# Optimization experiments

Hardware: AMD Instinct MI355X
Metric: run time of the kernel (lower is better)

## Reference

```python
import jax, jax.numpy as jnp
import numpy as np
import math

B, T, C = 4, 2048, 2048
H, D = 16, 128
DH = D // 2  # 64 rotation planes
OMEGA_SCALE = 16.0
EPS = 1e-5


def setup_inputs() -> dict:
    key = jax.random.key(0)
    ks = jax.random.split(key, 8)
    w_std = 1.0 / math.sqrt(C)
    x = jax.random.normal(ks[0], (B, T, C), dtype=jnp.float32)
    Wq = jax.random.normal(ks[1], (C, C), dtype=jnp.float32) * w_std
    Wk = jax.random.normal(ks[2], (C, C), dtype=jnp.float32) * w_std
    Wv = jax.random.normal(ks[3], (C, C), dtype=jnp.float32) * w_std
    # c_proj init std = 0.5/sqrt(n_embd)/sqrt(n_layer), n_layer=24
    Wo = jax.random.normal(ks[4], (C, C), dtype=jnp.float32) * (0.5 / math.sqrt(C) / math.sqrt(24))
    # omega_proj: weight init zeros, bias = softplus_inverse(0.001); perturb weight slightly for a nontrivial phase
    w_omega = jax.random.normal(ks[5], (1, C), dtype=jnp.float32) * 0.01
    b_omega = jnp.full((1,), math.log(math.expm1(0.001)), dtype=jnp.float32)
    # log_freq initialized from RoPE inverse frequencies, base 10000
    inv_freq = 1.0 / (10000.0 ** (np.arange(0, D, 2, dtype=np.float32) / D))
    log_freq = jnp.asarray(np.log(inv_freq), dtype=jnp.float32)
    q_gamma = jnp.ones((D,), dtype=jnp.float32)
    k_gamma = jnp.ones((D,), dtype=jnp.float32)
    return {"x": x, "Wq": Wq, "Wk": Wk, "Wv": Wv, "Wo": Wo,
            "w_omega": w_omega, "b_omega": b_omega, "log_freq": log_freq,
            "q_gamma": q_gamma, "k_gamma": k_gamma}


def _rmsnorm(t, gamma):
    return t * jax.lax.rsqrt(jnp.mean(t * t, axis=-1, keepdims=True) + EPS) * gamma


def reference(x, Wq, Wk, Wv, Wo, w_omega, b_omega, log_freq, q_gamma, k_gamma):
    # cumulative contextual phase: omega = sigmoid(omega_proj(x)/scale); phi_t = sum_{tau<t} omega_tau
    omega = jax.nn.sigmoid((x @ w_omega.T + b_omega).astype(jnp.float32) / OMEGA_SCALE)  # (B,T,1)
    phi = jnp.cumsum(omega, axis=1) - omega                                              # (B,T,1)

    q = (x @ Wq.T).reshape(B, T, H, D)
    k = (x @ Wk.T).reshape(B, T, H, D)
    v = (x @ Wv.T).reshape(B, T, H, D)

    # shared-across-heads frequencies theta_j; angles (B,T,1,DH) broadcast over heads
    freq = jnp.exp(log_freq)                       # (DH,)
    angles = phi[..., None] * freq                 # (B,T,1,DH)
    cos = jnp.cos(angles)
    sin = jnp.sin(angles)

    def rotate(t):
        t1, t2 = t[..., :DH], t[..., DH:]
        return jnp.concatenate([t1 * cos + t2 * sin, -t1 * sin + t2 * cos], axis=-1)

    q = rotate(q)
    k = rotate(k)
    q = _rmsnorm(q, q_gamma)
    k = _rmsnorm(k, k_gamma)

    # causal SDPA, scale 1/sqrt(D)
    scores = jnp.einsum('bthd,bshd->bhts', q, k) / math.sqrt(D)   # (B,H,T,T)
    mask = jnp.tril(jnp.ones((T, T), dtype=bool))
    scores = jnp.where(mask, scores, jnp.finfo(scores.dtype).min)
    probs = jax.nn.softmax(scores, axis=-1)
    y = jnp.einsum('bhts,bshd->bthd', probs, v)                   # (B,T,H,D)
    return y.reshape(B, T, H * D) @ Wo.T
```

## Files before the change

kernel.cpp:

```cpp
#include <hip/hip_runtime.h>
#include <math.h>

typedef __bf16 bf16;
typedef __bf16 bf16x8 __attribute__((ext_vector_type(8)));
typedef __bf16 bf16x4v __attribute__((ext_vector_type(4)));
typedef float f32x4 __attribute__((ext_vector_type(4)));

#define NB 4
#define NT 2048
#define NC 2048
#define NH 16
#define ND 128
#define NROW (NB*NT)

#define GLD16(g, l) __builtin_amdgcn_global_load_lds( \
    (__attribute__((address_space(1))) void*)(g), \
    (__attribute__((address_space(3))) void*)(l), 16, 0, 0)

__global__ void cvtx_omega_kernel(const float* __restrict__ x, bf16* __restrict__ xb,
                                  const float* __restrict__ w_om, const float* __restrict__ b_om,
                                  float* __restrict__ omega) {
  int row = blockIdx.x;
  const float4* xr = reinterpret_cast<const float4*>(x + (size_t)row * NC);
  const float4* wr = reinterpret_cast<const float4*>(w_om);
  bf16x4v* ob = reinterpret_cast<bf16x4v*>(xb + (size_t)row * NC);
  float sum = 0.f;
  for (int i = threadIdx.x; i < NC/4; i += 256) {
    float4 a = xr[i], b = wr[i];
    sum += a.x*b.x + a.y*b.y + a.z*b.z + a.w*b.w;
    bf16x4v o;
    o[0] = (bf16)a.x; o[1] = (bf16)a.y; o[2] = (bf16)a.z; o[3] = (bf16)a.w;
    ob[i] = o;
  }
  for (int m = 32; m; m >>= 1) sum += __shfl_xor(sum, m);
  __shared__ float wsum[4];
  if ((threadIdx.x & 63) == 0) wsum[threadIdx.x >> 6] = sum;
  __syncthreads();
  if (threadIdx.x == 0) {
    float d = wsum[0] + wsum[1] + wsum[2] + wsum[3] + b_om[0];
    omega[row] = 1.f / (1.f + expf(-d * (1.f/16.f)));
  }
}

__global__ void cvt_kernel(const float* __restrict__ in, bf16* __restrict__ out, int n4) {
  int stride = gridDim.x * blockDim.x;
  for (int i = blockIdx.x * blockDim.x + threadIdx.x; i < n4; i += stride) {
    float4 v = reinterpret_cast<const float4*>(in)[i];
    bf16x4v o;
    o[0] = (bf16)v.x; o[1] = (bf16)v.y; o[2] = (bf16)v.z; o[3] = (bf16)v.w;
    reinterpret_cast<bf16x4v*>(out)[i] = o;
  }
}

__global__ void scan_kernel(const float* __restrict__ omega, float* __restrict__ phi) {
  int b = blockIdx.x;
  const float* om = omega + (size_t)b * NT;
  float* ph = phi + (size_t)b * NT;
  int t = threadIdx.x;
  float v[8]; float s = 0.f;
  #pragma unroll
  for (int j = 0; j < 8; j++) { v[j] = om[t*8 + j]; s += v[j]; }
  __shared__ float totals[256];
  __shared__ double base_sh[256];
  totals[t] = s;
  __syncthreads();
  if (t == 0) {
    double run = 0.0;
    for (int i = 0; i < 256; i++) { base_sh[i] = run; run += (double)totals[i]; }
  }
  __syncthreads();
  double run = base_sh[t];
  #pragma unroll
  for (int j = 0; j < 8; j++) { ph[t*8 + j] = (float)run; run += (double)v[j]; }
}

__global__ void sincos_kernel(const float* __restrict__ phi, const float* __restrict__ log_freq,
                              float* __restrict__ cos_t, float* __restrict__ sin_t) {
  int i = blockIdx.x * 256 + threadIdx.x;
  int row = i >> 6, dd = i & 63;
  float f = expf(log_freq[dd]);
  float a = phi[row] * f;
  float si, co;
  sincosf(a, &si, &co);
  cos_t[i] = co;
  sin_t[i] = si;
}

template<int MODE>
__global__ __launch_bounds__(512, 2)
void gemm256(const bf16* __restrict__ Ag, const bf16* __restrict__ Bg,
             void* __restrict__ Cout,
             const float* __restrict__ cos_t, const float* __restrict__ sin_t,
             const float* __restrict__ gamma, float outscale) {
  constexpr int NKT = NC / 64;
  __shared__ bf16 Als[2][256 * 64];
  __shared__ bf16 Bls[2][256 * 64];
  const int t = threadIdx.x;
  const int lane = t & 63, lg = lane >> 4, l15 = lane & 15;
  const int wid = t >> 6, wm = wid >> 1, wn = wid & 1;
  const int bid = blockIdx.x;
  const int wg = (bid & 7) * 32 + (bid >> 3);
  const int m0 = (wg >> 3) * 256, n0 = (wg & 7) * 256;

  const size_t K2 = (size_t)NC * 2;
  const int scol = ((t & 7) * 16) ^ (((t >> 3) & 7) << 4);
  const char* aS = (const char*)Ag + (size_t)(m0 + (t >> 3)) * K2 + scol;
  const char* bS = (const char*)Bg + (size_t)(n0 + (t >> 3)) * K2 + scol;

  const int colk0 = (lg * 16) ^ ((l15 & 7) << 4);
  const int colk[2] = { colk0, colk0 ^ 64 };
  const int arow = (wm * 64 + l15) * 128;
  const int brow = (wn * 128 + l15) * 128;

  f32x4 acc[4][8] = {};

#define STAGE_TA(kt, d) do { \
    const char* sa_ = aS + (size_t)(kt) * 128; \
    char* da_ = (char*)&Als[d][0] + t * 16; \
    GLD16(sa_,            da_); \
    GLD16(sa_ +  64*K2,   da_ + 8192); \
    GLD16(sa_ + 128*K2,   da_ + 16384); \
    GLD16(sa_ + 192*K2,   da_ + 24576); \
  } while(0)
#define STAGE_TB(kt, d) do { \
    const char* sb_ = bS + (size_t)(kt) * 128; \
    char* db_ = (char*)&Bls[d][0] + t * 16; \
    GLD16(sb_,            db_); \
    GLD16(sb_ +  64*K2,   db_ + 8192); \
    GLD16(sb_ + 128*K2,   db_ + 16384); \
    GLD16(sb_ + 192*K2,   db_ + 24576); \
  } while(0)

  STAGE_TA(0, 0); STAGE_TB(0, 0);
  asm volatile("s_waitcnt vmcnt(0)" ::: "memory");
  __builtin_amdgcn_s_barrier();
  asm volatile("" ::: "memory");

  bf16x8 aC[2][2], bC[4][2];
  for (int kt = 0; kt < NKT; kt++) {
    const int d = kt & 1;
    const char* Ab = (const char*)&Als[d][0];
    const char* Bb = (const char*)&Bls[d][0];
    const bool pf = (kt + 1 < NKT);

    #pragma unroll
    for (int i = 0; i < 2; i++)
      #pragma unroll
      for (int kk = 0; kk < 2; kk++)
        aC[i][kk] = *(const bf16x8*)(Ab + arow + (i*16)*128 + colk[kk]);
    #pragma unroll
    for (int j = 0; j < 4; j++)
      #pragma unroll
      for (int kk = 0; kk < 2; kk++)
        bC[j][kk] = *(const bf16x8*)(Bb + brow + (j*16)*128 + colk[kk]);
    if (pf) STAGE_TA(kt+1, d^1);
    __builtin_amdgcn_s_barrier();
    asm volatile("s_waitcnt lgkmcnt(0)");
    __builtin_amdgcn_s_setprio(1);
    #pragma unroll
    for (int kk = 0; kk < 2; kk++)
      #pragma unroll
      for (int i = 0; i < 2; i++)
        #pragma unroll
        for (int j = 0; j < 4; j++)
          acc[i][j] = __builtin_amdgcn_mfma_f32_16x16x32_bf16(aC[i][kk], bC[j][kk], acc[i][j], 0,0,0);
    __builtin_amdgcn_s_setprio(0);

    #pragma unroll
    for (int i = 0; i < 2; i++)
      #pragma unroll
      for (int kk = 0; kk < 2; kk++)
        aC[i][kk] = *(const bf16x8*)(Ab + arow + ((32 + i*16))*128 + colk[kk]);
    if (pf) STAGE_TB(kt+1, d^1);
    __builtin_amdgcn_s_barrier();
    asm volatile("s_waitcnt lgkmcnt(0)");
    __builtin_amdgcn_s_setprio(1);
    #pragma unroll
    for (int kk = 0; kk < 2; kk++)
      #pragma unroll
      for (int i = 0; i < 2; i++)
        #pragma unroll
        for (int j = 0; j < 4; j++)
          acc[2+i][j] = __builtin_amdgcn_mfma_f32_16x16x32_bf16(aC[i][kk], bC[j][kk], acc[2+i][j], 0,0,0);
    __builtin_amdgcn_s_setprio(0);

    #pragma unroll
    for (int j = 0; j < 4; j++)
      #pragma unroll
      for (int kk = 0; kk < 2; kk++)
        bC[j][kk] = *(const bf16x8*)(Bb + brow + ((64 + j*16))*128 + colk[kk]);
    __builtin_amdgcn_s_barrier();
    asm volatile("s_waitcnt lgkmcnt(0)");
    __builtin_amdgcn_s_setprio(1);
    #pragma unroll
    for (int kk = 0; kk < 2; kk++)
      #pragma unroll
      for (int i = 0; i < 2; i++)
        #pragma unroll
        for (int j = 0; j < 4; j++)
          acc[2+i][4+j] = __builtin_amdgcn_mfma_f32_16x16x32_bf16(aC[i][kk], bC[j][kk], acc[2+i][4+j], 0,0,0);
    __builtin_amdgcn_s_setprio(0);

    #pragma unroll
    for (int i = 0; i < 2; i++)
      #pragma unroll
      for (int kk = 0; kk < 2; kk++)
        aC[i][kk] = *(const bf16x8*)(Ab + arow + (i*16)*128 + colk[kk]);
    __builtin_amdgcn_s_barrier();
    asm volatile("s_waitcnt lgkmcnt(0)");
    __builtin_amdgcn_s_setprio(1);
    #pragma unroll
    for (int kk = 0; kk < 2; kk++)
      #pragma unroll
      for (int i = 0; i < 2; i++)
        #pragma unroll
        for (int j = 0; j < 4; j++)
          acc[i][4+j] = __builtin_amdgcn_mfma_f32_16x16x32_bf16(aC[i][kk], bC[j][kk], acc[i][4+j], 0,0,0);
    __builtin_amdgcn_s_setprio(0);

    asm volatile("s_waitcnt vmcnt(0)" ::: "memory");
    __builtin_amdgcn_s_barrier();
    asm volatile("" ::: "memory");
  }
#undef STAGE_TA
#undef STAGE_TB

  if constexpr (MODE == 0) {
    bf16* out = (bf16*)Cout;
    #pragma unroll
    for (int mi = 0; mi < 4; mi++) {
      #pragma unroll
      for (int r = 0; r < 4; r++) {
        int m = m0 + wm*64 + mi*16 + lg*4 + r;
        float ss = 0.f;
        #pragma unroll
        for (int nj = 0; nj < 8; nj++) { float v = acc[mi][nj][r]; ss += v*v; }
        ss += __shfl_xor(ss, 1); ss += __shfl_xor(ss, 2);
        ss += __shfl_xor(ss, 4); ss += __shfl_xor(ss, 8);
        float scale = rsqrtf(ss * (1.f/128.f) + 1e-5f) * outscale;
        size_t rowb = (size_t)m * NC + n0 + wn*128;
        size_t tabb = (size_t)m * 64;
        #pragma unroll
        for (int nj = 0; nj < 4; nj++) {
          int dd = nj*16 + l15;
          float c = cos_t[tabb + dd];
          float s = sin_t[tabb + dd];
          float t1 = acc[mi][nj][r], t2 = acc[mi][nj+4][r];
          float o1 = (t1*c + t2*s) * scale * gamma[dd];
          float o2 = (t2*c - t1*s) * scale * gamma[dd + 64];
          out[rowb + dd] = (bf16)o1;
          out[rowb + dd + 64] = (bf16)o2;
        }
      }
    }
  } else if constexpr (MODE == 1) {
    bf16* vt = (bf16*)Cout;
    const int h = (n0 + wn*128) >> 7;
    #pragma unroll
    for (int mi = 0; mi < 4; mi++) {
      #pragma unroll
      for (int r = 0; r < 4; r++) {
        int m = m0 + wm*64 + mi*16 + lg*4 + r;
        int bidx = m >> 11, tt = m & (NT-1);
        size_t hb = (((size_t)bidx * NH + h) * ND) * NT + tt;
        #pragma unroll
        for (int nj = 0; nj < 8; nj++) {
          int d = nj*16 + l15;
          vt[hb + (size_t)d * NT] = (bf16)acc[mi][nj][r];
        }
      }
    }
  } else {
    float* out = (float*)Cout;
    #pragma unroll
    for (int mi = 0; mi < 4; mi++) {
      #pragma unroll
      for (int r = 0; r < 4; r++) {
        int m = m0 + wm*64 + mi*16 + lg*4 + r;
        size_t rowb = (size_t)m * NC + n0 + wn*128;
        #pragma unroll
        for (int nj = 0; nj < 8; nj++)
          out[rowb + nj*16 + l15] = acc[mi][nj][r];
      }
    }
  }
}

__global__ __launch_bounds__(512, 2)
void fa_kernel(const bf16* __restrict__ Qg, const bf16* __restrict__ Kg,
               const bf16* __restrict__ Vt, bf16* __restrict__ Og) {
  __shared__ bf16 Kls[2][64 * 128];
  __shared__ bf16 Vls[128 * 64];
  __shared__ bf16 Pls[8][32 * 64];
  const int t = threadIdx.x, w = t >> 6, lane = t & 63, lg = lane >> 4, l15 = lane & 15;
  const int bh = blockIdx.x;
  const int qb = (gridDim.y - 1) - blockIdx.y;
  const size_t qkbase = (size_t)(bh >> 4) * NT * NC + (size_t)(bh & 15) * ND;
  const size_t vbase  = (size_t)bh * ND * NT;
  const int q0 = qb * 256 + w * 32;

  bf16x8 qf[2][4];
  #pragma unroll
  for (int mt = 0; mt < 2; mt++)
    #pragma unroll
    for (int kc = 0; kc < 4; kc++)
      qf[mt][kc] = *reinterpret_cast<const bf16x8*>(
          Qg + qkbase + (size_t)(q0 + mt*16 + l15) * NC + kc*32 + lg*8);

  f32x4 oacc[2][8] = {};
  f32x4 lacc[2] = {};
  float m_run[2][4];
  #pragma unroll
  for (int mt = 0; mt < 2; mt++)
    #pragma unroll
    for (int r = 0; r < 4; r++) m_run[mt][r] = -1e30f;

  bf16x8 vone;
  #pragma unroll
  for (int i = 0; i < 8; i++) vone[i] = (bf16)1.0f;

  const int kinS = ((t & 15) * 16) ^ (((t >> 4) & 7) << 4);
  const char* ksrc0 = (const char*)(Kg + qkbase) + (size_t)(t >> 4) * (NC*2) + kinS;
  const int vinS = ((t & 7) * 16) ^ (((t >> 3) & 7) << 4);
  const char* vsrc0 = (const char*)(Vt + vbase) + (size_t)(t >> 3) * (NT*2) + vinS;

#define STAGE_K(kt, dd) do { \
    const char* ks_ = ksrc0 + (size_t)(kt) * 64 * (NC*2); \
    char* kd_ = (char*)&Kls[dd][0] + t * 16; \
    GLD16(ks_,                        kd_); \
    GLD16(ks_ + (size_t)32 * NC * 2,  kd_ + 8192); \
  } while(0)
#define STAGE_V(kt) do { \
    const char* vs_ = vsrc0 + (size_t)(kt) * 128; \
    char* vd_ = (char*)&Vls[0] + t * 16; \
    GLD16(vs_,                        vd_); \
    GLD16(vs_ + (size_t)64 * NT * 2,  vd_ + 8192); \
  } while(0)

  const int ntiles = 4 * qb + 4;
  STAGE_K(0, 0);
  __syncthreads();

  for (int kt = 0; kt < ntiles; kt++) {
    const int d = kt & 1;
    const int kv0 = kt * 64;
    if (kt + 1 < ntiles) STAGE_K(kt + 1, d ^ 1);
    STAGE_V(kt);

    const bool active = (q0 + 31 >= kv0);
    if (active) {
      f32x4 s[2][4] = {};
      __builtin_amdgcn_s_setprio(1);
      #pragma unroll
      for (int kc = 0; kc < 4; kc++) {
        bf16x8 kf[4];
        const int swz = ((kc*64 + lg*16) ^ ((l15 & 7) << 4));
        #pragma unroll
        for (int nt = 0; nt < 4; nt++)
          kf[nt] = *reinterpret_cast<const bf16x8*>((const char*)&Kls[d][0] + (nt*16 + l15) * 256 + swz);
        #pragma unroll
        for (int mt = 0; mt < 2; mt++)
          #pragma unroll
          for (int nt = 0; nt < 4; nt++)
            s[mt][nt] = __builtin_amdgcn_mfma_f32_16x16x32_bf16(qf[mt][kc], kf[nt], s[mt][nt], 0, 0, 0);
      }
      __builtin_amdgcn_s_setprio(0);

      if (kv0 + 63 > q0) {
        #pragma unroll
        for (int mt = 0; mt < 2; mt++)
          #pragma unroll
          for (int nt = 0; nt < 4; nt++) {
            int kv = kv0 + nt*16 + l15;
            #pragma unroll
            for (int r = 0; r < 4; r++)
              if (kv > q0 + mt*16 + lg*4 + r) s[mt][nt][r] = -1e30f;
          }
      }

      float tmax[2][4];
      #pragma unroll
      for (int mt = 0; mt < 2; mt++)
        #pragma unroll
        for (int r = 0; r < 4; r++) {
          float tm = fmaxf(fmaxf(s[mt][0][r], s[mt][1][r]), fmaxf(s[mt][2][r], s[mt][3][r]));
          tm = fmaxf(tm, __shfl_xor(tm, 1));
          tm = fmaxf(tm, __shfl_xor(tm, 2));
          tm = fmaxf(tm, __shfl_xor(tm, 4));
          tm = fmaxf(tm, __shfl_xor(tm, 8));
          tmax[mt][r] = tm;
        }

      int ok = 1;
      #pragma unroll
      for (int mt = 0; mt < 2; mt++)
        #pragma unroll
        for (int r = 0; r < 4; r++) ok &= (tmax[mt][r] <= m_run[mt][r] + 8.0f);
      if (!__all(ok)) {
        #pragma unroll
        for (int mt = 0; mt < 2; mt++) {
          f32x4 alv;
          #pragma unroll
          for (int r = 0; r < 4; r++) {
            float mn = fmaxf(m_run[mt][r], tmax[mt][r]);
            alv[r] = exp2f(m_run[mt][r] - mn);
            m_run[mt][r] = mn;
          }
          #pragma unroll
          for (int dt = 0; dt < 8; dt++) {
            f32x4 o = oacc[mt][dt];
            o[0] *= alv[0]; o[1] *= alv[1]; o[2] *= alv[2]; o[3] *= alv[3];
            oacc[mt][dt] = o;
          }
          f32x4 lv = lacc[mt];
          lv[0] *= alv[0]; lv[1] *= alv[1]; lv[2] *= alv[2]; lv[3] *= alv[3];
          lacc[mt] = lv;
        }
      }

      char* pw = (char*)&Pls[w][0];
      #pragma unroll
      for (int mt = 0; mt < 2; mt++)
        #pragma unroll
        for (int r = 0; r < 4; r++) {
          float p0 = exp2f(s[mt][0][r] - m_run[mt][r]);
          float p1 = exp2f(s[mt][1][r] - m_run[mt][r]);
          float p2 = exp2f(s[mt][2][r] - m_run[mt][r]);
          float p3 = exp2f(s[mt][3][r] - m_run[mt][r]);
          int qrow = mt*16 + lg*4 + r;
          int rb = qrow * 128, cX = (qrow & 7) << 4;
          *(bf16*)(pw + rb + ((       2*l15) ^ cX)) = (bf16)p0;
          *(bf16*)(pw + rb + (( 32 +  2*l15) ^ cX)) = (bf16)p1;
          *(bf16*)(pw + rb + (( 64 +  2*l15) ^ cX)) = (bf16)p2;
          *(bf16*)(pw + rb + (( 96 +  2*l15) ^ cX)) = (bf16)p3;
        }
    }

    asm volatile("s_waitcnt vmcnt(0)" ::: "memory");
    __builtin_amdgcn_s_barrier();
    asm volatile("" ::: "memory");

    if (active) {
      char* pw = (char*)&Pls[w][0];
      bf16x8 pf[2][2];
      #pragma unroll
      for (int mt = 0; mt < 2; mt++)
        #pragma unroll
        for (int kc2 = 0; kc2 < 2; kc2++)
          pf[mt][kc2] = *reinterpret_cast<const bf16x8*>(
              pw + (mt*16 + l15) * 128 + ((kc2*64 + lg*16) ^ ((l15 & 7) << 4)));
      __builtin_amdgcn_s_setprio(1);
      #pragma unroll
      for (int kc2 = 0; kc2 < 2; kc2++) {
        #pragma unroll
        for (int mt = 0; mt < 2; mt++)
          lacc[mt] = __builtin_amdgcn_mfma_f32_16x16x32_bf16(pf[mt][kc2], vone, lacc[mt], 0, 0, 0);
        const int swz = ((kc2*64 + lg*16) ^ ((l15 & 7) << 4));
        #pragma unroll
        for (int dt = 0; dt < 8; dt++) {
          bf16x8 vf = *reinterpret_cast<const bf16x8*>((const char*)&Vls[0] + (dt*16 + l15) * 128 + swz);
          #pragma unroll
          for (int mt = 0; mt < 2; mt++)
            oacc[mt][dt] = __builtin_amdgcn_mfma_f32_16x16x32_bf16(pf[mt][kc2], vf, oacc[mt][dt], 0, 0, 0);
        }
      }
      __builtin_amdgcn_s_setprio(0);
    }

    __syncthreads();
  }
#undef STAGE_K
#undef STAGE_V

  #pragma unroll
  for (int mt = 0; mt < 2; mt++)
    #pragma unroll
    for (int r = 0; r < 4; r++) {
      float inv = 1.f / lacc[mt][r];
      size_t orow = qkbase + (size_t)(q0 + mt*16 + lg*4 + r) * NC;
      #pragma unroll
      for (int dt = 0; dt < 8; dt++)
        Og[orow + dt*16 + l15] = (bf16)(oacc[mt][dt][r] * inv);
    }
}

extern "C" void kernel_launch(void* const* d_in, const int* in_sizes, int n_in,
                              void* d_out, int out_size, void* d_ws, size_t ws_size,
                              hipStream_t stream) {
  (void)in_sizes; (void)n_in; (void)out_size; (void)ws_size;
  const float* x       = (const float*)d_in[0];
  const float* Wq      = (const float*)d_in[1];
  const float* Wk      = (const float*)d_in[2];
  const float* Wv      = (const float*)d_in[3];
  const float* Wo      = (const float*)d_in[4];
  const float* w_omega = (const float*)d_in[5];
  const float* b_omega = (const float*)d_in[6];
  const float* log_freq= (const float*)d_in[7];
  const float* q_gamma = (const float*)d_in[8];
  const float* k_gamma = (const float*)d_in[9];

  char* p = (char*)d_ws;
  auto alloc = [&](size_t bytes) { void* r = (void*)p; p += (bytes + 255) & ~(size_t)255; return r; };
  bf16* xb   = (bf16*)alloc((size_t)NROW * NC * 2);
  bf16* wqb  = (bf16*)alloc((size_t)NC * NC * 2);
  bf16* wkb  = (bf16*)alloc((size_t)NC * NC * 2);
  bf16* wvb  = (bf16*)alloc((size_t)NC * NC * 2);
  bf16* wob  = (bf16*)alloc((size_t)NC * NC * 2);
  bf16* qb   = (bf16*)alloc((size_t)NROW * NC * 2);
  bf16* kb   = (bf16*)alloc((size_t)NROW * NC * 2);
  bf16* vt   = (bf16*)alloc((size_t)NROW * NC * 2);
  bf16* ob   = (bf16*)alloc((size_t)NROW * NC * 2);
  float* omega = (float*)alloc((size_t)NROW * 4);
  float* phi   = (float*)alloc((size_t)NROW * 4);
  float* cos_t = (float*)alloc((size_t)NROW * 64 * 4);
  float* sin_t = (float*)alloc((size_t)NROW * 64 * 4);

  cvtx_omega_kernel<<<NROW, 256, 0, stream>>>(x, xb, w_omega, b_omega, omega);
  cvt_kernel<<<2048, 256, 0, stream>>>(Wq, wqb, NC * NC / 4);
  cvt_kernel<<<2048, 256, 0, stream>>>(Wk, wkb, NC * NC / 4);
  cvt_kernel<<<2048, 256, 0, stream>>>(Wv, wvb, NC * NC / 4);
  cvt_kernel<<<2048, 256, 0, stream>>>(Wo, wob, NC * NC / 4);
  scan_kernel<<<NB, 256, 0, stream>>>(omega, phi);
  sincos_kernel<<<NROW * 64 / 256, 256, 0, stream>>>(phi, log_freq, cos_t, sin_t);

  const float sc2 = 0.12751726f;
  gemm256<0><<<256, 512, 0, stream>>>(xb, wqb, qb, cos_t, sin_t, q_gamma, sc2);
  gemm256<0><<<256, 512, 0, stream>>>(xb, wkb, kb, cos_t, sin_t, k_gamma, 1.0f);
  gemm256<1><<<256, 512, 0, stream>>>(xb, wvb, vt, nullptr, nullptr, nullptr, 1.0f);

  fa_kernel<<<dim3(NB * NH, NT / 256), 512, 0, stream>>>(qb, kb, vt, ob);

  gemm256<2><<<256, 512, 0, stream>>>(ob, wob, d_out, nullptr, nullptr, nullptr, 1.0f);
}
```

Before: 473.3 us.

## Split GEMM tile loads into four quarter stages with finer vmcnt waits

```diff
diff --git a/kernel.cpp b/kernel.cpp
--- a/kernel.cpp
+++ b/kernel.cpp
@@ -42,14 +42,18 @@
   }
 }
 
-__global__ void cvt_kernel(const float* __restrict__ in, bf16* __restrict__ out, int n4) {
-  int stride = gridDim.x * blockDim.x;
-  for (int i = blockIdx.x * blockDim.x + threadIdx.x; i < n4; i += stride) {
-    float4 v = reinterpret_cast<const float4*>(in)[i];
-    bf16x4v o;
-    o[0] = (bf16)v.x; o[1] = (bf16)v.y; o[2] = (bf16)v.z; o[3] = (bf16)v.w;
-    reinterpret_cast<bf16x4v*>(out)[i] = o;
-  }
+__global__ void cvtw_kernel(const float* __restrict__ W0, const float* __restrict__ W1,
+                            const float* __restrict__ W2, const float* __restrict__ W3,
+                            bf16* __restrict__ o0, bf16* __restrict__ o1,
+                            bf16* __restrict__ o2, bf16* __restrict__ o3) {
+  int which = blockIdx.x >> 12;
+  const float* in = which == 0 ? W0 : which == 1 ? W1 : which == 2 ? W2 : W3;
+  bf16* out = which == 0 ? o0 : which == 1 ? o1 : which == 2 ? o2 : o3;
+  int i = (blockIdx.x & 4095) * 256 + threadIdx.x;
+  float4 v = reinterpret_cast<const float4*>(in)[i];
+  bf16x4v o;
+  o[0] = (bf16)v.x; o[1] = (bf16)v.y; o[2] = (bf16)v.z; o[3] = (bf16)v.w;
+  reinterpret_cast<bf16x4v*>(out)[i] = o;
 }
 
 __global__ void scan_kernel(const float* __restrict__ omega, float* __restrict__ phi) {
@@ -103,127 +107,146 @@
   const int m0 = (wg >> 3) * 256, n0 = (wg & 7) * 256;
 
   const size_t K2 = (size_t)NC * 2;
-  const int scol = ((t & 7) * 16) ^ (((t >> 3) & 7) << 4);
-  const char* aS = (const char*)Ag + (size_t)(m0 + (t >> 3)) * K2 + scol;
-  const char* bS = (const char*)Bg + (size_t)(n0 + (t >> 3)) * K2 + scol;
+  const int tr = t >> 3;
+  const int scol = ((t & 7) * 16) ^ ((tr & 7) << 4);
+  const int mA_g0 = ((tr >> 5) * 64) + (tr & 31);
+  const int mA_g1 = (((64 + tr) >> 5) * 64) + ((64 + tr) & 31);
+  const char* a1s0 = (const char*)Ag + (size_t)(m0 + mA_g0) * K2 + scol;
+  const char* a1s1 = (const char*)Ag + (size_t)(m0 + mA_g1) * K2 + scol;
+  const char* a3s0 = (const char*)Ag + (size_t)(m0 + mA_g0 + 32) * K2 + scol;
+  const char* a3s1 = (const char*)Ag + (size_t)(m0 + mA_g1 + 32) * K2 + scol;
+  const char* b2s0 = (const char*)Bg + (size_t)(n0 + tr) * K2 + scol;
+  const char* b2s1 = (const char*)Bg + (size_t)(n0 + 128 + tr) * K2 + scol;
+  const char* b4s0 = (const char*)Bg + (size_t)(n0 + 64 + tr) * K2 + scol;
+  const char* b4s1 = (const char*)Bg + (size_t)(n0 + 192 + tr) * K2 + scol;
 
   const int colk0 = (lg * 16) ^ ((l15 & 7) << 4);
-  const int colk[2] = { colk0, colk0 ^ 64 };
-  const int arow = (wm * 64 + l15) * 128;
-  const int brow = (wn * 128 + l15) * 128;
+  const int colk1 = colk0 ^ 64;
+  int arowL[4], browL[8];
+  #pragma unroll
+  for (int mi = 0; mi < 4; mi++)
+    arowL[mi] = (((mi >> 1) * 128) + wm * 32 + ((mi & 1) * 16) + l15) * 128;
+  #pragma unroll
+  for (int nj = 0; nj < 8; nj++)
+    browL[nj] = (((nj >> 2) * 128) + wn * 64 + ((nj & 3) * 16) + l15) * 128;
 
   f32x4 acc[4][8] = {};
 
-#define STAGE_TA(kt, d) do { \
-    const char* sa_ = aS + (size_t)(kt) * 128; \
-    char* da_ = (char*)&Als[d][0] + t * 16; \
-    GLD16(sa_,            da_); \
-    GLD16(sa_ +  64*K2,   da_ + 8192); \
-    GLD16(sa_ + 128*K2,   da_ + 16384); \
-    GLD16(sa_ + 192*K2,   da_ + 24576); \
+#define STAGE_S1(kt, dd) do { char* _d = (char*)&Als[dd][0] + t * 16; \
+    GLD16(a1s0 + (size_t)(kt) * 128, _d); GLD16(a1s1 + (size_t)(kt) * 128, _d + 8192); } while(0)
+#define STAGE_S2(kt, dd) do { char* _d = (char*)&Bls[dd][0] + t * 16; \
+    GLD16(b2s0 + (size_t)(kt) * 128, _d); GLD16(b2s1 + (size_t)(kt) * 128, _d + 8192); } while(0)
+#define STAGE_S3(kt, dd) do { char* _d = (char*)&Als[dd][0] + 16384 + t * 16; \
+    GLD16(a3s0 + (size_t)(kt) * 128, _d); GLD16(a3s1 + (size_t)(kt) * 128, _d + 8192); } while(0)
+#define STAGE_S4(kt, dd) do { char* _d = (char*)&Bls[dd][0] + 16384 + t * 16; \
+    GLD16(b4s0 + (size_t)(kt) * 128, _d); GLD16(b4s1 + (size_t)(kt) * 128, _d + 8192); } while(0)
+
+#define MFMA16(IB, JB) do { \
+    _Pragma("unroll") \
+    for (int kk = 0; kk < 2; kk++) \
+      _Pragma("unroll") \
+      for (int i = 0; i < 2; i++) \
+        _Pragma("unroll") \
+        for (int j = 0; j < 4; j++) \
+          acc[(IB)+i][(JB)+j] = __builtin_amdgcn_mfma_f32_16x16x32_bf16(aC[i][kk], bC[j][kk], acc[(IB)+i][(JB)+j], 0,0,0); \
   } while(0)
-#define STAGE_TB(kt, d) do { \
-    const char* sb_ = bS + (size_t)(kt) * 128; \
-    char* db_ = (char*)&Bls[d][0] + t * 16; \
-    GLD16(sb_,            db_); \
-    GLD16(sb_ +  64*K2,   db_ + 8192); \
-    GLD16(sb_ + 128*K2,   db_ + 16384); \
-    GLD16(sb_ + 192*K2,   db_ + 24576); \
+
+#define RD_A(mibase) do { \
+    _Pragma("unroll") \
+    for (int i = 0; i < 2; i++) { \
+      aC[i][0] = *(const bf16x8*)(Ab + arowL[(mibase)+i] + colk0); \
+      aC[i][1] = *(const bf16x8*)(Ab + arowL[(mibase)+i] + colk1); } \
   } while(0)
-
-  STAGE_TA(0, 0); STAGE_TB(0, 0);
-  asm volatile("s_waitcnt vmcnt(0)" ::: "memory");
+#define RD_B(njbase) do { \
+    _Pragma("unroll") \
+    for (int j = 0; j < 4; j++) { \
+      bC[j][0] = *(const bf16x8*)(Bb + browL[(njbase)+j] + colk0); \
+      bC[j][1] = *(const bf16x8*)(Bb + browL[(njbase)+j] + colk1); } \
+  } while(0)
+
+  STAGE_S1(0, 0); STAGE_S2(0, 0); STAGE_S3(0, 0); STAGE_S4(0, 0);
+  asm volatile("s_waitcnt vmcnt(4)" ::: "memory");
   __builtin_amdgcn_s_barrier();
   asm volatile("" ::: "memory");
 
   bf16x8 aC[2][2], bC[4][2];
-  for (int kt = 0; kt < NKT; kt++) {
+  for (int kt = 0; kt < NKT - 1; kt++) {
     const int d = kt & 1;
     const char* Ab = (const char*)&Als[d][0];
     const char* Bb = (const char*)&Bls[d][0];
-    const bool pf = (kt + 1 < NKT);
-
-    #pragma unroll
-    for (int i = 0; i < 2; i++)
-      #pragma unroll
-      for (int kk = 0; kk < 2; kk++)
-        aC[i][kk] = *(const bf16x8*)(Ab + arow + (i*16)*128 + colk[kk]);
-    #pragma unroll
-    for (int j = 0; j < 4; j++)
-      #pragma unroll
-      for (int kk = 0; kk < 2; kk++)
-        bC[j][kk] = *(const bf16x8*)(Bb + brow + (j*16)*128 + colk[kk]);
-    if (pf) STAGE_TA(kt+1, d^1);
-    __builtin_amdgcn_s_barrier();
-    asm volatile("s_waitcnt lgkmcnt(0)");
+
+    RD_A(0); RD_B(0);
+    STAGE_S1(kt + 1, d ^ 1);
+    asm volatile("s_waitcnt vmcnt(4)" ::: "memory");
+    __builtin_amdgcn_s_barrier();
+    asm volatile("s_waitcnt lgkmcnt(0)" ::: "memory");
     __builtin_amdgcn_s_setprio(1);
-    #pragma unroll
-    for (int kk = 0; kk < 2; kk++)
-      #pragma unroll
-      for (int i = 0; i < 2; i++)
-        #pragma unroll
-        for (int j = 0; j < 4; j++)
-          acc[i][j] = __builtin_amdgcn_mfma_f32_16x16x32_bf16(aC[i][kk], bC[j][kk], acc[i][j], 0,0,0);
+    MFMA16(0, 0);
     __builtin_amdgcn_s_setprio(0);
-
-    #pragma unroll
-    for (int i = 0; i < 2; i++)
-      #pragma unroll
-      for (int kk = 0; kk < 2; kk++)
-        aC[i][kk] = *(const bf16x8*)(Ab + arow + ((32 + i*16))*128 + colk[kk]);
-    if (pf) STAGE_TB(kt+1, d^1);
-    __builtin_amdgcn_s_barrier();
-    asm volatile("s_waitcnt lgkmcnt(0)");
+    __builtin_amdgcn_s_barrier();
+
+    RD_A(2);
+    STAGE_S2(kt + 1, d ^ 1);
+    asm volatile("s_waitcnt vmcnt(4)" ::: "memory");
+    __builtin_amdgcn_s_barrier();
+    asm volatile("s_waitcnt lgkmcnt(0)" ::: "memory");
     __builtin_amdgcn_s_setprio(1);
-    #pragma unroll
-    for (int kk = 0; kk < 2; kk++)
-      #pragma unroll
-      for (int i = 0; i < 2; i++)
-        #pragma unroll
-        for (int j = 0; j < 4; j++)
-          acc[2+i][j] = __builtin_amdgcn_mfma_f32_16x16x32_bf16(aC[i][kk], bC[j][kk], acc[2+i][j], 0,0,0);
+    MFMA16(2, 0);
     __builtin_amdgcn_s_setprio(0);
-
-    #pragma unroll
-    for (int j = 0; j < 4; j++)
-      #pragma unroll
-      for (int kk = 0; kk < 2; kk++)
-        bC[j][kk] = *(const bf16x8*)(Bb + brow + ((64 + j*16))*128 + colk[kk]);
-    __builtin_amdgcn_s_barrier();
-    asm volatile("s_waitcnt lgkmcnt(0)");
+    __builtin_amdgcn_s_barrier();
+
+    RD_B(4);
+    STAGE_S3(kt + 1, d ^ 1);
+    __builtin_amdgcn_s_barrier();
+    asm volatile("s_waitcnt lgkmcnt(0)" ::: "memory");
     __builtin_amdgcn_s_setprio(1);
-    #pragma unroll
-    for (int kk = 0; kk < 2; kk++)
-      #pragma unroll
-      for (int i = 0; i < 2; i++)
-        #pragma unroll
-        for (int j = 0; j < 4; j++)
-          acc[2+i][4+j] = __builtin_amdgcn_mfma_f32_16x16x32_bf16(aC[i][kk], bC[j][kk], acc[2+i][4+j], 0,0,0);
+    MFMA16(2, 4);
     __builtin_amdgcn_s_setprio(0);
-
-    #pragma unroll
-    for (int i = 0; i < 2; i++)
-      #pragma unroll
-      for (int kk = 0; kk < 2; kk++)
-        aC[i][kk] = *(const bf16x8*)(Ab + arow + (i*16)*128 + colk[kk]);
-    __builtin_amdgcn_s_barrier();
-    asm volatile("s_waitcnt lgkmcnt(0)");
+    __builtin_amdgcn_s_barrier();
+
+    RD_A(0);
+    STAGE_S4(kt + 1, d ^ 1);
+    asm volatile("s_waitcnt vmcnt(4)" ::: "memory");
+    __builtin_amdgcn_s_barrier();
+    asm volatile("s_waitcnt lgkmcnt(0)" ::: "memory");
     __builtin_amdgcn_s_setprio(1);
-    #pragma unroll
-    for (int kk = 0; kk < 2; kk++)
-      #pragma unroll
-      for (int i = 0; i < 2; i++)
-        #pragma unroll
-        for (int j = 0; j < 4; j++)
-          acc[i][4+j] = __builtin_amdgcn_mfma_f32_16x16x32_bf16(aC[i][kk], bC[j][kk], acc[i][4+j], 0,0,0);
+    MFMA16(0, 4);
     __builtin_amdgcn_s_setprio(0);
-
+    __builtin_amdgcn_s_barrier();
+  }
+
+  {
+    const int d = (NKT - 1) & 1;
+    const char* Ab = (const char*)&Als[d][0];
+    const char* Bb = (const char*)&Bls[d][0];
+    RD_A(0); RD_B(0);
     asm volatile("s_waitcnt vmcnt(0)" ::: "memory");
     __builtin_amdgcn_s_barrier();
-    asm volatile("" ::: "memory");
-  }
-#undef STAGE_TA
-#undef STAGE_TB
+    asm volatile("s_waitcnt lgkmcnt(0)" ::: "memory");
+    MFMA16(0, 0);
+    __builtin_amdgcn_s_barrier();
+    RD_A(2);
+    __builtin_amdgcn_s_barrier();
+    asm volatile("s_waitcnt lgkmcnt(0)" ::: "memory");
+    MFMA16(2, 0);
+    __builtin_amdgcn_s_barrier();
+    RD_B(4);
+    __builtin_amdgcn_s_barrier();
+    asm volatile("s_waitcnt lgkmcnt(0)" ::: "memory");
+    MFMA16(2, 4);
+    __builtin_amdgcn_s_barrier();
+    RD_A(0);
+    __builtin_amdgcn_s_barrier();
+    asm volatile("s_waitcnt lgkmcnt(0)" ::: "memory");
+    MFMA16(0, 4);
+  }
+#undef STAGE_S1
+#undef STAGE_S2
+#undef STAGE_S3
+#undef STAGE_S4
+#undef MFMA16
+#undef RD_A
+#undef RD_B
 
   if constexpr (MODE == 0) {
     bf16* out = (bf16*)Cout;
@@ -516,10 +539,7 @@
   float* sin_t = (float*)alloc((size_t)NROW * 64 * 4);
 
   cvtx_omega_kernel<<<NROW, 256, 0, stream>>>(x, xb, w_omega, b_omega, omega);
-  cvt_kernel<<<2048, 256, 0, stream>>>(Wq, wqb, NC * NC / 4);
-  cvt_kernel<<<2048, 256, 0, stream>>>(Wk, wkb, NC * NC / 4);
-  cvt_kernel<<<2048, 256, 0, stream>>>(Wv, wvb, NC * NC / 4);
-  cvt_kernel<<<2048, 256, 0, stream>>>(Wo, wob, NC * NC / 4);
+  cvtw_kernel<<<16384, 256, 0, stream>>>(Wq, Wk, Wv, Wo, wqb, wkb, wvb, wob);
   scan_kernel<<<NB, 256, 0, stream>>>(omega, phi);
   sincos_kernel<<<NROW * 64 / 256, 256, 0, stream>>>(phi, log_freq, cos_t, sin_t);
 
```

Result: slower. 511.8 us (+8.1%).

## Double-buffer V tiles in flash attention and merge weight conversion kernels

Applied to the files above, without the earlier changes.

```diff
diff --git a/kernel.cpp b/kernel.cpp
--- a/kernel.cpp
+++ b/kernel.cpp
@@ -42,14 +42,18 @@
   }
 }
 
-__global__ void cvt_kernel(const float* __restrict__ in, bf16* __restrict__ out, int n4) {
-  int stride = gridDim.x * blockDim.x;
-  for (int i = blockIdx.x * blockDim.x + threadIdx.x; i < n4; i += stride) {
-    float4 v = reinterpret_cast<const float4*>(in)[i];
-    bf16x4v o;
-    o[0] = (bf16)v.x; o[1] = (bf16)v.y; o[2] = (bf16)v.z; o[3] = (bf16)v.w;
-    reinterpret_cast<bf16x4v*>(out)[i] = o;
-  }
+__global__ void cvtw_kernel(const float* __restrict__ W0, const float* __restrict__ W1,
+                            const float* __restrict__ W2, const float* __restrict__ W3,
+                            bf16* __restrict__ o0, bf16* __restrict__ o1,
+                            bf16* __restrict__ o2, bf16* __restrict__ o3) {
+  int which = blockIdx.x >> 12;
+  const float* in = which == 0 ? W0 : which == 1 ? W1 : which == 2 ? W2 : W3;
+  bf16* out = which == 0 ? o0 : which == 1 ? o1 : which == 2 ? o2 : o3;
+  int i = (blockIdx.x & 4095) * 256 + threadIdx.x;
+  float4 v = reinterpret_cast<const float4*>(in)[i];
+  bf16x4v o;
+  o[0] = (bf16)v.x; o[1] = (bf16)v.y; o[2] = (bf16)v.z; o[3] = (bf16)v.w;
+  reinterpret_cast<bf16x4v*>(out)[i] = o;
 }
 
 __global__ void scan_kernel(const float* __restrict__ omega, float* __restrict__ phi) {
@@ -290,7 +294,7 @@
 void fa_kernel(const bf16* __restrict__ Qg, const bf16* __restrict__ Kg,
                const bf16* __restrict__ Vt, bf16* __restrict__ Og) {
   __shared__ bf16 Kls[2][64 * 128];
-  __shared__ bf16 Vls[128 * 64];
+  __shared__ bf16 Vls[2][128 * 64];
   __shared__ bf16 Pls[8][32 * 64];
   const int t = threadIdx.x, w = t >> 6, lane = t & 63, lg = lane >> 4, l15 = lane & 15;
   const int bh = blockIdx.x;
@@ -324,31 +328,29 @@
   const int vinS = ((t & 7) * 16) ^ (((t >> 3) & 7) << 4);
   const char* vsrc0 = (const char*)(Vt + vbase) + (size_t)(t >> 3) * (NT*2) + vinS;
 
-#define STAGE_K(kt, dd) do { \
+#define STAGE_KV(kt, dd) do { \
     const char* ks_ = ksrc0 + (size_t)(kt) * 64 * (NC*2); \
+    const char* vs_ = vsrc0 + (size_t)(kt) * 128; \
     char* kd_ = (char*)&Kls[dd][0] + t * 16; \
+    char* vd_ = (char*)&Vls[dd][0] + t * 16; \
     GLD16(ks_,                        kd_); \
     GLD16(ks_ + (size_t)32 * NC * 2,  kd_ + 8192); \
-  } while(0)
-#define STAGE_V(kt) do { \
-    const char* vs_ = vsrc0 + (size_t)(kt) * 128; \
-    char* vd_ = (char*)&Vls[0] + t * 16; \
     GLD16(vs_,                        vd_); \
     GLD16(vs_ + (size_t)64 * NT * 2,  vd_ + 8192); \
   } while(0)
 
   const int ntiles = 4 * qb + 4;
-  STAGE_K(0, 0);
-  __syncthreads();
+  STAGE_KV(0, 0);
+  asm volatile("s_waitcnt vmcnt(0)" ::: "memory");
+  __builtin_amdgcn_s_barrier();
+  asm volatile("" ::: "memory");
 
   for (int kt = 0; kt < ntiles; kt++) {
     const int d = kt & 1;
     const int kv0 = kt * 64;
-    if (kt + 1 < ntiles) STAGE_K(kt + 1, d ^ 1);
-    STAGE_V(kt);
-
-    const bool active = (q0 + 31 >= kv0);
-    if (active) {
+    if (kt + 1 < ntiles) STAGE_KV(kt + 1, d ^ 1);
+
+    if (q0 + 31 >= kv0) {
       f32x4 s[2][4] = {};
       __builtin_amdgcn_s_setprio(1);
       #pragma unroll
@@ -434,14 +436,9 @@
           *(bf16*)(pw + rb + (( 64 +  2*l15) ^ cX)) = (bf16)p2;
           *(bf16*)(pw + rb + (( 96 +  2*l15) ^ cX)) = (bf16)p3;
         }
-    }
-
-    asm volatile("s_waitcnt vmcnt(0)" ::: "memory");
-    __builtin_amdgcn_s_barrier();
-    asm volatile("" ::: "memory");
-
-    if (active) {
-      char* pw = (char*)&Pls[w][0];
+
+      asm volatile("s_waitcnt lgkmcnt(0)" ::: "memory");
+
       bf16x8 pf[2][2];
       #pragma unroll
       for (int mt = 0; mt < 2; mt++)
@@ -458,7 +455,7 @@
         const int swz = ((kc2*64 + lg*16) ^ ((l15 & 7) << 4));
         #pragma unroll
         for (int dt = 0; dt < 8; dt++) {
-          bf16x8 vf = *reinterpret_cast<const bf16x8*>((const char*)&Vls[0] + (dt*16 + l15) * 128 + swz);
+          bf16x8 vf = *reinterpret_cast<const bf16x8*>((const char*)&Vls[d][0] + (dt*16 + l15) * 128 + swz);
           #pragma unroll
           for (int mt = 0; mt < 2; mt++)
             oacc[mt][dt] = __builtin_amdgcn_mfma_f32_16x16x32_bf16(pf[mt][kc2], vf, oacc[mt][dt], 0, 0, 0);
@@ -467,10 +464,11 @@
       __builtin_amdgcn_s_setprio(0);
     }
 
-    __syncthreads();
+    asm volatile("s_waitcnt vmcnt(0)" ::: "memory");
+    __builtin_amdgcn_s_barrier();
+    asm volatile("" ::: "memory");
   }
-#undef STAGE_K
-#undef STAGE_V
+#undef STAGE_KV
 
   #pragma unroll
   for (int mt = 0; mt < 2; mt++)
@@ -516,10 +514,7 @@
   float* sin_t = (float*)alloc((size_t)NROW * 64 * 4);
 
   cvtx_omega_kernel<<<NROW, 256, 0, stream>>>(x, xb, w_omega, b_omega, omega);
-  cvt_kernel<<<2048, 256, 0, stream>>>(Wq, wqb, NC * NC / 4);
-  cvt_kernel<<<2048, 256, 0, stream>>>(Wk, wkb, NC * NC / 4);
-  cvt_kernel<<<2048, 256, 0, stream>>>(Wv, wvb, NC * NC / 4);
-  cvt_kernel<<<2048, 256, 0, stream>>>(Wo, wob, NC * NC / 4);
+  cvtw_kernel<<<16384, 256, 0, stream>>>(Wq, Wk, Wv, Wo, wqb, wkb, wvb, wob);
   scan_kernel<<<NB, 256, 0, stream>>>(omega, phi);
   sincos_kernel<<<NROW * 64 / 256, 256, 0, stream>>>(phi, log_freq, cos_t, sin_t);
 
```

Result: faster. 462.8 us (-2.2%).
